# Optimization experiments

Hardware: AMD Instinct MI355X
Metric: run time of the kernel (lower is better)

The kernel has to match this reference:

```python
import jax, jax.numpy as jnp
import numpy as np

N_NODES = 50000
N_EDGES = 1600000
N_OBS = 128
HIDDEN = 128
N_ACT = 32
K_OUT = 64


def gcn_conv(x, W, b, src, dst, n_nodes):
    """PyG GCNConv: out = D^{-1/2} (A + I) D^{-1/2} (x W) + b.

    Self-loop handled analytically (norm = 1/deg for the loop edge)
    instead of concatenating loop edges.
    """
    h = x @ W  # [N, out]
    # degree with self loops: in-degree + 1
    deg = jnp.zeros((n_nodes,), x.dtype).at[dst].add(jnp.ones((), x.dtype)) + 1.0
    dinv = jax.lax.rsqrt(deg)  # deg >= 1, safe
    norm = dinv[src] * dinv[dst]  # [E]
    agg = jax.ops.segment_sum(h[src] * norm[:, None], dst, num_segments=n_nodes)
    agg = agg + h * (dinv * dinv)[:, None]  # self-loop term: h / deg
    return agg + b


def setup_inputs() -> dict:
    key = jax.random.key(0)
    ks = jax.random.split(key, 6)
    x = jax.random.normal(ks[0], (N_OBS, N_NODES), dtype=jnp.float32)
    edge_index = jax.random.randint(ks[1], (2, N_EDGES), 0, N_NODES, dtype=jnp.int64)
    onehot_values = jax.random.uniform(ks[2], (K_OUT, N_NODES), dtype=jnp.float32)
    W1 = jax.random.normal(ks[3], (N_OBS, HIDDEN), dtype=jnp.float32) / np.sqrt(N_OBS)
    b1 = jnp.zeros((HIDDEN,), jnp.float32)
    W2 = jax.random.normal(ks[4], (HIDDEN, N_ACT), dtype=jnp.float32) / np.sqrt(HIDDEN)
    b2 = jnp.zeros((N_ACT,), jnp.float32)
    return {"x": x, "edge_index": edge_index, "onehot_values": onehot_values,
            "W1": W1, "b1": b1, "W2": W2, "b2": b2}


def reference(x, edge_index, onehot_values, W1, b1, W2, b2):
    # eval mode: dropout is identity
    src, dst = edge_index[0], edge_index[1]
    h = x.T  # graph.x.T -> [N, n_obs]
    h = jax.nn.relu(gcn_conv(h, W1, b1, src, dst, N_NODES))
    h = gcn_conv(h, W2, b2, src, dst, N_NODES)
    return onehot_values @ h  # [K_OUT, N_ACT]
```

## Files before the change

kernel.cpp:

```cpp
#include <hip/hip_runtime.h>

#define NN 50000
#define NE 1600000
#define NB 98
#define BSH 9
#define BCAP 17408

#define OFF_H1    0
#define OFF_AGG1  3200000
#define OFF_HW2   9600000
#define OFF_AGG2  10400000
#define OFF_DINV  12000000
#define OFF_ROWS  12050000
#define OFF_GCNT  12101000
#define OFF_GBASE 12101200
#define OFF_CSRC  12102000
#define OFF_BIN   13702000

typedef __attribute__((ext_vector_type(8))) short bf16x8;
typedef __attribute__((ext_vector_type(8))) unsigned short u16x8;
typedef __attribute__((ext_vector_type(4))) float f32x4;

__device__ __forceinline__ unsigned short f2b(float f) {
    unsigned u = __float_as_uint(f);
    u += 0x7fffu + ((u >> 16) & 1u);
    return (unsigned short)(u >> 16);
}
__device__ __forceinline__ float b2f(unsigned short h) {
    return __uint_as_float((unsigned)h << 16);
}
__device__ __forceinline__ float blo(unsigned u) { return __uint_as_float(u << 16); }
__device__ __forceinline__ float bhi(unsigned u) { return __uint_as_float(u & 0xffff0000u); }

__global__ __launch_bounds__(256) void k_binA(const int* __restrict__ ei,
                                              int* __restrict__ gcount,
                                              unsigned* __restrict__ binned) {
    __shared__ int hist[NB];
    const int t = threadIdx.x;
    if (t < NB) hist[t] = 0;
    __syncthreads();
    const int e0 = blockIdx.x * (NE / 256);
    const int e1 = e0 + (NE / 256);
    for (int e = e0 + t; e < e1; e += 256)
        atomicAdd(&hist[ei[NE + e] >> BSH], 1);
    __syncthreads();
    if (t < NB) {
        const int v = hist[t];
        hist[t] = atomicAdd(&gcount[t], v);
    }
    __syncthreads();
    for (int e = e0 + t; e < e1; e += 256) {
        const int s = ei[e], d = ei[NE + e];
        const int b = d >> BSH;
        const int pos = atomicAdd(&hist[b], 1);
        binned[(size_t)b * BCAP + pos] = (unsigned)s | ((unsigned)(d & 511) << 16);
    }
}

__global__ __launch_bounds__(128) void k_base(const int* __restrict__ gcount,
                                              int* __restrict__ gbase) {
    __shared__ int s[128];
    const int t = threadIdx.x;
    const int v = (t < NB) ? gcount[t] : 0;
    s[t] = v;
    __syncthreads();
    #pragma unroll
    for (int off = 1; off < 128; off <<= 1) {
        const int x = (t >= off) ? s[t - off] : 0;
        __syncthreads();
        s[t] += x;
        __syncthreads();
    }
    if (t < NB) gbase[t] = s[t] - v;
    if (t == NB - 1) gbase[NB] = s[t];
}

__global__ __launch_bounds__(256) void k_binB(const int* __restrict__ gcount,
                                              const int* __restrict__ gbase,
                                              const unsigned* __restrict__ binned,
                                              int* __restrict__ rows,
                                              float* __restrict__ dinv,
                                              int* __restrict__ csrc) {
    __shared__ int deg[512];
    __shared__ int off[512];
    __shared__ int partial[256];
    const int b = blockIdx.x, t = threadIdx.x;
    const int n0 = b << BSH;
    const int nloc = (NN - n0 < 512) ? (NN - n0) : 512;
    const int cnt = gcount[b];
    const int obase = gbase[b];
    const unsigned* eb = binned + (size_t)b * BCAP;
    deg[t] = 0;
    deg[t + 256] = 0;
    __syncthreads();
    for (int i = t; i < cnt; i += 256) atomicAdd(&deg[eb[i] >> 16], 1);
    __syncthreads();
    const int s0 = deg[2 * t], s1 = deg[2 * t + 1];
    partial[t] = s0 + s1;
    __syncthreads();
    #pragma unroll
    for (int o = 1; o < 256; o <<= 1) {
        const int x = (t >= o) ? partial[t - o] : 0;
        __syncthreads();
        partial[t] += x;
        __syncthreads();
    }
    const int ep = partial[t] - (s0 + s1);
    off[2 * t] = ep;
    off[2 * t + 1] = ep + s0;
    __syncthreads();
    for (int i = t; i < nloc; i += 256) {
        rows[n0 + i] = obase + off[i];
        dinv[n0 + i] = rsqrtf((float)deg[i] + 1.0f);
    }
    if (b == NB - 1 && t == 0) rows[NN] = NE;
    __syncthreads();
    for (int i = t; i < cnt; i += 256) {
        const unsigned r = eb[i];
        const int local = atomicAdd(&off[r >> 16], 1);
        csrc[obase + local] = (int)(r & 0xffffu);
    }
}

__global__ __launch_bounds__(256) void k_w1t(const float* __restrict__ W1,
                                             unsigned short* __restrict__ w1t) {
    const int id = blockIdx.x * 1024 + threadIdx.x;
    #pragma unroll
    for (int i = 0; i < 4; ++i) {
        const int e = id + 256 * i;
        const int k = e >> 7, c = e & 127;
        w1t[c * 128 + k] = f2b(W1[e]);
    }
}

__global__ __launch_bounds__(256) void k_gemm1(const float* __restrict__ x,
                                               const unsigned short* __restrict__ w1t,
                                               const float* __restrict__ dinv,
                                               unsigned short* __restrict__ h1s) {
    __shared__ unsigned short lxs[64 * 136];
    const int t = threadIdx.x;
    const int gn0 = blockIdx.x * 64;
    {
        const int col = t & 63, kr = t >> 6;
        const int gn = gn0 + col;
        #pragma unroll
        for (int i = 0; i < 4; ++i) {
            const int k0 = kr * 32 + i * 8;
            u16x8 v;
            #pragma unroll
            for (int j = 0; j < 8; ++j) {
                const float xv = (gn < NN) ? x[(size_t)(k0 + j) * NN + gn] : 0.f;
                v[j] = f2b(xv);
            }
            *(u16x8*)&lxs[col * 136 + k0] = v;
        }
    }
    __syncthreads();
    const int w = t >> 6, l = t & 63;
    const int lr = l & 15, lg = l >> 4;
    const unsigned short* pa = &lxs[(w * 16 + lr) * 136 + lg * 8];
    f32x4 acc[8];
    #pragma unroll
    for (int ct = 0; ct < 8; ++ct) acc[ct] = (f32x4){0.f, 0.f, 0.f, 0.f};
    #pragma unroll
    for (int ks = 0; ks < 4; ++ks) {
        const bf16x8 av = *(const bf16x8*)&pa[ks * 32];
        const unsigned short* pw = &w1t[lr * 128 + ks * 32 + lg * 8];
        const bf16x8 b0 = *(const bf16x8*)&pw[0 * 16 * 128];
        const bf16x8 b1 = *(const bf16x8*)&pw[1 * 16 * 128];
        const bf16x8 b2 = *(const bf16x8*)&pw[2 * 16 * 128];
        const bf16x8 b3 = *(const bf16x8*)&pw[3 * 16 * 128];
        const bf16x8 b4 = *(const bf16x8*)&pw[4 * 16 * 128];
        const bf16x8 b5 = *(const bf16x8*)&pw[5 * 16 * 128];
        const bf16x8 b6 = *(const bf16x8*)&pw[6 * 16 * 128];
        const bf16x8 b7 = *(const bf16x8*)&pw[7 * 16 * 128];
        acc[0] = __builtin_amdgcn_mfma_f32_16x16x32_bf16(av, b0, acc[0], 0, 0, 0);
        acc[1] = __builtin_amdgcn_mfma_f32_16x16x32_bf16(av, b1, acc[1], 0, 0, 0);
        acc[2] = __builtin_amdgcn_mfma_f32_16x16x32_bf16(av, b2, acc[2], 0, 0, 0);
        acc[3] = __builtin_amdgcn_mfma_f32_16x16x32_bf16(av, b3, acc[3], 0, 0, 0);
        acc[4] = __builtin_amdgcn_mfma_f32_16x16x32_bf16(av, b4, acc[4], 0, 0, 0);
        acc[5] = __builtin_amdgcn_mfma_f32_16x16x32_bf16(av, b5, acc[5], 0, 0, 0);
        acc[6] = __builtin_amdgcn_mfma_f32_16x16x32_bf16(av, b6, acc[6], 0, 0, 0);
        acc[7] = __builtin_amdgcn_mfma_f32_16x16x32_bf16(av, b7, acc[7], 0, 0, 0);
    }
    __syncthreads();
    const int nl0 = w * 16 + lg * 4;
    const float4 dv = *(const float4*)&dinv[gn0 + nl0];
    const float dva[4] = {dv.x, dv.y, dv.z, dv.w};
    #pragma unroll
    for (int ct = 0; ct < 8; ++ct) {
        const int c = ct * 16 + lr;
        #pragma unroll
        for (int r = 0; r < 4; ++r)
            lxs[(nl0 + r) * 136 + c] = f2b(acc[ct][r] * dva[r]);
    }
    __syncthreads();
    {
        const int row = t >> 2, cb = (t & 3) * 32;
        const int gn = gn0 + row;
        if (gn < NN) {
            #pragma unroll
            for (int i = 0; i < 4; ++i)
                *(u16x8*)&h1s[(size_t)gn * 128 + cb + i * 8] =
                    *(const u16x8*)&lxs[row * 136 + cb + i * 8];
        }
    }
}

__global__ __launch_bounds__(256) void k_gather1(const int* __restrict__ rows,
                                                 const int* __restrict__ csrc,
                                                 const float* __restrict__ dinv,
                                                 const unsigned short* __restrict__ h1s,
                                                 unsigned short* __restrict__ ag1b) {
    const int n = __builtin_amdgcn_readfirstlane((blockIdx.x * 256 + threadIdx.x) >> 6);
    const int lane = threadIdx.x & 63;
    if (n >= NN) return;
    const int beg = rows[n], end = rows[n + 1];
    float ax0 = 0.f, ay0 = 0.f, ax1 = 0.f, ay1 = 0.f;
    float ax2 = 0.f, ay2 = 0.f, ax3 = 0.f, ay3 = 0.f;
    int p = beg;
    for (; p + 16 <= end; p += 16) {
        const int s0 = csrc[p + 0], s1 = csrc[p + 1], s2 = csrc[p + 2], s3 = csrc[p + 3];
        const int s4 = csrc[p + 4], s5 = csrc[p + 5], s6 = csrc[p + 6], s7 = csrc[p + 7];
        const int s8 = csrc[p + 8], s9 = csrc[p + 9], sa = csrc[p + 10], sb = csrc[p + 11];
        const int sc = csrc[p + 12], sd = csrc[p + 13], se = csrc[p + 14], sf = csrc[p + 15];
        const unsigned u0 = *(const unsigned*)&h1s[(size_t)s0 * 128 + lane * 2];
        const unsigned u1 = *(const unsigned*)&h1s[(size_t)s1 * 128 + lane * 2];
        const unsigned u2 = *(const unsigned*)&h1s[(size_t)s2 * 128 + lane * 2];
        const unsigned u3 = *(const unsigned*)&h1s[(size_t)s3 * 128 + lane * 2];
        const unsigned u4 = *(const unsigned*)&h1s[(size_t)s4 * 128 + lane * 2];
        const unsigned u5 = *(const unsigned*)&h1s[(size_t)s5 * 128 + lane * 2];
        const unsigned u6 = *(const unsigned*)&h1s[(size_t)s6 * 128 + lane * 2];
        const unsigned u7 = *(const unsigned*)&h1s[(size_t)s7 * 128 + lane * 2];
        const unsigned u8 = *(const unsigned*)&h1s[(size_t)s8 * 128 + lane * 2];
        const unsigned u9 = *(const unsigned*)&h1s[(size_t)s9 * 128 + lane * 2];
        const unsigned ua = *(const unsigned*)&h1s[(size_t)sa * 128 + lane * 2];
        const unsigned ub = *(const unsigned*)&h1s[(size_t)sb * 128 + lane * 2];
        const unsigned uc = *(const unsigned*)&h1s[(size_t)sc * 128 + lane * 2];
        const unsigned ud = *(const unsigned*)&h1s[(size_t)sd * 128 + lane * 2];
        const unsigned ue = *(const unsigned*)&h1s[(size_t)se * 128 + lane * 2];
        const unsigned uf = *(const unsigned*)&h1s[(size_t)sf * 128 + lane * 2];
        ax0 += blo(u0); ay0 += bhi(u0);
        ax1 += blo(u1); ay1 += bhi(u1);
        ax2 += blo(u2); ay2 += bhi(u2);
        ax3 += blo(u3); ay3 += bhi(u3);
        ax0 += blo(u4); ay0 += bhi(u4);
        ax1 += blo(u5); ay1 += bhi(u5);
        ax2 += blo(u6); ay2 += bhi(u6);
        ax3 += blo(u7); ay3 += bhi(u7);
        ax0 += blo(u8); ay0 += bhi(u8);
        ax1 += blo(u9); ay1 += bhi(u9);
        ax2 += blo(ua); ay2 += bhi(ua);
        ax3 += blo(ub); ay3 += bhi(ub);
        ax0 += blo(uc); ay0 += bhi(uc);
        ax1 += blo(ud); ay1 += bhi(ud);
        ax2 += blo(ue); ay2 += bhi(ue);
        ax3 += blo(uf); ay3 += bhi(uf);
    }
    for (; p + 4 <= end; p += 4) {
        const int s0 = csrc[p + 0], s1 = csrc[p + 1], s2 = csrc[p + 2], s3 = csrc[p + 3];
        const unsigned u0 = *(const unsigned*)&h1s[(size_t)s0 * 128 + lane * 2];
        const unsigned u1 = *(const unsigned*)&h1s[(size_t)s1 * 128 + lane * 2];
        const unsigned u2 = *(const unsigned*)&h1s[(size_t)s2 * 128 + lane * 2];
        const unsigned u3 = *(const unsigned*)&h1s[(size_t)s3 * 128 + lane * 2];
        ax0 += blo(u0); ay0 += bhi(u0);
        ax1 += blo(u1); ay1 += bhi(u1);
        ax2 += blo(u2); ay2 += bhi(u2);
        ax3 += blo(u3); ay3 += bhi(u3);
    }
    for (; p < end; ++p) {
        const int s = csrc[p];
        const unsigned u0 = *(const unsigned*)&h1s[(size_t)s * 128 + lane * 2];
        ax0 += blo(u0); ay0 += bhi(u0);
    }
    const float dn = dinv[n];
    const float sx = ((ax0 + ax1) + (ax2 + ax3)) * dn;
    const float sy = ((ay0 + ay1) + (ay2 + ay3)) * dn;
    const unsigned pk = (unsigned)f2b(sx) | ((unsigned)f2b(sy) << 16);
    *(unsigned*)&ag1b[(size_t)n * 128 + lane * 2] = pk;
}

__global__ __launch_bounds__(256) void k_fuse1(const unsigned short* __restrict__ ag1b,
                                               const unsigned short* __restrict__ h1s,
                                               const float* __restrict__ dinv,
                                               const float* __restrict__ b1,
                                               const float* __restrict__ W2,
                                               unsigned short* __restrict__ hw2s) {
    __shared__ float hs[32][132];
    __shared__ float w2s[128 * 32];
    const int t = threadIdx.x;
    const int n0 = blockIdx.x * 32;
    #pragma unroll
    for (int i = 0; i < 16; ++i) w2s[t + 256 * i] = W2[t + 256 * i];
    #pragma unroll
    for (int i = 0; i < 4; ++i) {
        const int idx4 = t + 256 * i;
        const int n = idx4 >> 5, c4 = (idx4 & 31) * 4;
        const int node = n0 + n;
        float4 r = make_float4(0.f, 0.f, 0.f, 0.f);
        if (node < NN) {
            const ushort4 au = *(const ushort4*)&ag1b[(size_t)node * 128 + c4];
            const ushort4 hu = *(const ushort4*)&h1s[(size_t)node * 128 + c4];
            const float dn = dinv[node];
            const float4 bb = *(const float4*)&b1[c4];
            r.x = fmaxf(fmaf(b2f(hu.x), dn, b2f(au.x)) + bb.x, 0.f);
            r.y = fmaxf(fmaf(b2f(hu.y), dn, b2f(au.y)) + bb.y, 0.f);
            r.z = fmaxf(fmaf(b2f(hu.z), dn, b2f(au.z)) + bb.z, 0.f);
            r.w = fmaxf(fmaf(b2f(hu.w), dn, b2f(au.w)) + bb.w, 0.f);
        }
        *(float4*)&hs[n][c4] = r;
    }
    __syncthreads();
    const int n = t >> 3, j4 = (t & 7) * 4;
    const int node = n0 + n;
    float acc[4] = {0.f, 0.f, 0.f, 0.f};
    #pragma unroll 8
    for (int k = 0; k < 128; ++k) {
        const float hv = hs[n][k];
        const float4 wv = *(const float4*)&w2s[k * 32 + j4];
        acc[0] = fmaf(hv, wv.x, acc[0]);
        acc[1] = fmaf(hv, wv.y, acc[1]);
        acc[2] = fmaf(hv, wv.z, acc[2]);
        acc[3] = fmaf(hv, wv.w, acc[3]);
    }
    if (node < NN) {
        const float ds = dinv[node];
        ushort4 pk;
        pk.x = f2b(acc[0] * ds); pk.y = f2b(acc[1] * ds);
        pk.z = f2b(acc[2] * ds); pk.w = f2b(acc[3] * ds);
        *(ushort4*)&hw2s[(size_t)node * 32 + j4] = pk;
    }
}

__global__ __launch_bounds__(256) void k_gather2(const int* __restrict__ rows,
                                                 const int* __restrict__ csrc,
                                                 const float* __restrict__ dinv,
                                                 const unsigned short* __restrict__ hw2s,
                                                 float* __restrict__ agg2) {
    const int n = __builtin_amdgcn_readfirstlane((blockIdx.x * 256 + threadIdx.x) >> 6);
    const int lane = threadIdx.x & 63;
    const int j = lane & 31;
    const int hi = lane >> 5;
    if (n >= NN) return;
    const int beg = rows[n], end = rows[n + 1];
    float a0 = 0.f, a1 = 0.f, a2 = 0.f, a3 = 0.f;
    float a4 = 0.f, a5 = 0.f, a6 = 0.f, a7 = 0.f;
    int p = beg;
    for (; p + 16 <= end; p += 16) {
        const int e0 = csrc[p + 0 + hi],  e1 = csrc[p + 2 + hi];
        const int e2 = csrc[p + 4 + hi],  e3 = csrc[p + 6 + hi];
        const int e4 = csrc[p + 8 + hi],  e5 = csrc[p + 10 + hi];
        const int e6 = csrc[p + 12 + hi], e7 = csrc[p + 14 + hi];
        const unsigned short v0 = hw2s[(size_t)e0 * 32 + j];
        const unsigned short v1 = hw2s[(size_t)e1 * 32 + j];
        const unsigned short v2 = hw2s[(size_t)e2 * 32 + j];
        const unsigned short v3 = hw2s[(size_t)e3 * 32 + j];
        const unsigned short v4 = hw2s[(size_t)e4 * 32 + j];
        const unsigned short v5 = hw2s[(size_t)e5 * 32 + j];
        const unsigned short v6 = hw2s[(size_t)e6 * 32 + j];
        const unsigned short v7 = hw2s[(size_t)e7 * 32 + j];
        a0 += b2f(v0); a1 += b2f(v1); a2 += b2f(v2); a3 += b2f(v3);
        a4 += b2f(v4); a5 += b2f(v5); a6 += b2f(v6); a7 += b2f(v7);
    }
    for (; p + 2 <= end; p += 2) {
        const int e = csrc[p + hi];
        a0 += b2f(hw2s[(size_t)e * 32 + j]);
    }
    if (p < end) {
        if (!hi) {
            const int e = csrc[p];
            a0 += b2f(hw2s[(size_t)e * 32 + j]);
        }
    }
    float sum = ((a0 + a1) + (a2 + a3)) + ((a4 + a5) + (a6 + a7));
    sum += __shfl_xor(sum, 32);
    if (!hi) agg2[(size_t)n * 32 + j] = sum * dinv[n];
}

__global__ __launch_bounds__(256) void k_final(const float* __restrict__ O,
                                               const float* __restrict__ agg2,
                                               const unsigned short* __restrict__ hw2s,
                                               const float* __restrict__ dinv,
                                               const float* __restrict__ b2,
                                               float* __restrict__ out) {
    __shared__ float h2s[128][32];
    __shared__ float Os[64][128];
    const int t = threadIdx.x;
    const int n0 = blockIdx.x * 128;
    #pragma unroll
    for (int i = 0; i < 16; ++i) {
        const int idx = t + 256 * i;
        const int n = idx >> 5, j = idx & 31;
        const int node = n0 + n;
        float v = 0.f;
        if (node < NN) {
            const float dn = dinv[node];
            v = fmaf(b2f(hw2s[(size_t)node * 32 + j]), dn,
                     agg2[(size_t)node * 32 + j]) + b2[j];
        }
        h2s[n][j] = v;
    }
    #pragma unroll
    for (int i = 0; i < 32; ++i) {
        const int idx = t + 256 * i;
        const int r = idx >> 7, c = idx & 127;
        const int node = n0 + c;
        Os[r][c] = (node < NN) ? O[(size_t)r * NN + node] : 0.f;
    }
    __syncthreads();
    const int j = t & 31, k0 = (t >> 5) * 8;
    float acc[8];
    #pragma unroll
    for (int i = 0; i < 8; ++i) acc[i] = 0.f;
    for (int n = 0; n < 128; ++n) {
        const float hv = h2s[n][j];
        #pragma unroll
        for (int i = 0; i < 8; ++i) acc[i] = fmaf(Os[k0 + i][n], hv, acc[i]);
    }
    #pragma unroll
    for (int i = 0; i < 8; ++i) atomicAdd(&out[(k0 + i) * 32 + j], acc[i]);
}

extern "C" void kernel_launch(void* const* d_in, const int* in_sizes, int n_in,
                              void* d_out, int out_size, void* d_ws, size_t ws_size,
                              hipStream_t stream) {
    const float* x  = (const float*)d_in[0];
    const int*   ei = (const int*)d_in[1];
    const float* O  = (const float*)d_in[2];
    const float* W1 = (const float*)d_in[3];
    const float* b1 = (const float*)d_in[4];
    const float* W2 = (const float*)d_in[5];
    const float* b2 = (const float*)d_in[6];
    float* out = (float*)d_out;

    float* wsf = (float*)d_ws;
    unsigned short* h1s  = (unsigned short*)(wsf + OFF_H1);
    unsigned short* ag1b = (unsigned short*)(wsf + OFF_AGG1);
    unsigned short* hw2s = (unsigned short*)(wsf + OFF_HW2);
    float*          agg2 = wsf + OFF_AGG2;
    float* dinv  = wsf + OFF_DINV;
    int*   rows  = (int*)(wsf + OFF_ROWS);
    int*   gcnt  = (int*)(wsf + OFF_GCNT);
    int*   gbase = (int*)(wsf + OFF_GBASE);
    int*   csrc  = (int*)(wsf + OFF_CSRC);
    unsigned* binned = (unsigned*)(wsf + OFF_BIN);
    unsigned short* w1t = (unsigned short*)(wsf + OFF_BIN);

    hipMemsetAsync(gcnt, 0, NB * 4, stream);

    k_binA<<<256, 256, 0, stream>>>(ei, gcnt, binned);
    k_base<<<1, 128, 0, stream>>>(gcnt, gbase);
    k_binB<<<NB, 256, 0, stream>>>(gcnt, gbase, binned, rows, dinv, csrc);

    k_w1t<<<16, 256, 0, stream>>>(W1, w1t);
    k_gemm1<<<(NN + 63) / 64, 256, 0, stream>>>(x, w1t, dinv, h1s);
    k_gather1<<<(NN * 64 + 255) / 256, 256, 0, stream>>>(rows, csrc, dinv, h1s, ag1b);
    k_fuse1<<<(NN + 31) / 32, 256, 0, stream>>>(ag1b, h1s, dinv, b1, W2, hw2s);
    k_gather2<<<(NN * 64 + 255) / 256, 256, 0, stream>>>(rows, csrc, dinv, hw2s, agg2);

    hipMemsetAsync(out, 0, (size_t)out_size * 4, stream);
    k_final<<<(NN + 127) / 128, 256, 0, stream>>>(O, agg2, hw2s, dinv, b2, out);
}
```

Measured before the change: 219.4 us.

## Store CSR sources as 16-bit and split layer-1 gather into column halves

CSR source indices are stored as unsigned shorts and read as packed pairs, so each half-wave takes alternate edges. This halves the index bandwidth in both gathers. The layer-1 gather is split into two launches, each covering 64 feature columns with a cross-half shuffle reduction, to shrink the per-pass working set. The cost is an extra launch, indices read twice, and the assumption that node ids fit in 16 bits.

```diff
diff --git a/kernel.cpp b/kernel.cpp
--- a/kernel.cpp
+++ b/kernel.cpp
@@ -80,7 +80,7 @@
                                               const unsigned* __restrict__ binned,
                                               int* __restrict__ rows,
                                               float* __restrict__ dinv,
-                                              int* __restrict__ csrc) {
+                                              unsigned short* __restrict__ csrc) {
     __shared__ int deg[512];
     __shared__ int off[512];
     __shared__ int partial[256];
@@ -118,7 +118,7 @@
     for (int i = t; i < cnt; i += 256) {
         const unsigned r = eb[i];
         const int local = atomicAdd(&off[r >> 16], 1);
-        csrc[obase + local] = (int)(r & 0xffffu);
+        csrc[obase + local] = (unsigned short)(r & 0xffffu);
     }
 }
 
@@ -208,76 +208,82 @@
 }
 
 __global__ __launch_bounds__(256) void k_gather1(const int* __restrict__ rows,
-                                                 const int* __restrict__ csrc,
+                                                 const unsigned short* __restrict__ csrc,
                                                  const float* __restrict__ dinv,
                                                  const unsigned short* __restrict__ h1s,
-                                                 unsigned short* __restrict__ ag1b) {
+                                                 unsigned short* __restrict__ ag1b,
+                                                 const int coff) {
     const int n = __builtin_amdgcn_readfirstlane((blockIdx.x * 256 + threadIdx.x) >> 6);
     const int lane = threadIdx.x & 63;
     if (n >= NN) return;
+    const int j2 = (lane & 31) * 2;
+    const int hi = lane >> 5;
     const int beg = rows[n], end = rows[n + 1];
-    float ax0 = 0.f, ay0 = 0.f, ax1 = 0.f, ay1 = 0.f;
-    float ax2 = 0.f, ay2 = 0.f, ax3 = 0.f, ay3 = 0.f;
+    float a0x = 0.f, a0y = 0.f, a1x = 0.f, a1y = 0.f;
+    float a2x = 0.f, a2y = 0.f, a3x = 0.f, a3y = 0.f;
     int p = beg;
+    if ((p & 1) && p < end) {
+        if (!hi) {
+            const int s = csrc[p];
+            const unsigned u = *(const unsigned*)&h1s[(size_t)s * 128 + coff + j2];
+            a0x += blo(u); a0y += bhi(u);
+        }
+        ++p;
+    }
     for (; p + 16 <= end; p += 16) {
-        const int s0 = csrc[p + 0], s1 = csrc[p + 1], s2 = csrc[p + 2], s3 = csrc[p + 3];
-        const int s4 = csrc[p + 4], s5 = csrc[p + 5], s6 = csrc[p + 6], s7 = csrc[p + 7];
-        const int s8 = csrc[p + 8], s9 = csrc[p + 9], sa = csrc[p + 10], sb = csrc[p + 11];
-        const int sc = csrc[p + 12], sd = csrc[p + 13], se = csrc[p + 14], sf = csrc[p + 15];
-        const unsigned u0 = *(const unsigned*)&h1s[(size_t)s0 * 128 + lane * 2];
-        const unsigned u1 = *(const unsigned*)&h1s[(size_t)s1 * 128 + lane * 2];
-        const unsigned u2 = *(const unsigned*)&h1s[(size_t)s2 * 128 + lane * 2];
-        const unsigned u3 = *(const unsigned*)&h1s[(size_t)s3 * 128 + lane * 2];
-        const unsigned u4 = *(const unsigned*)&h1s[(size_t)s4 * 128 + lane * 2];
-        const unsigned u5 = *(const unsigned*)&h1s[(size_t)s5 * 128 + lane * 2];
-        const unsigned u6 = *(const unsigned*)&h1s[(size_t)s6 * 128 + lane * 2];
-        const unsigned u7 = *(const unsigned*)&h1s[(size_t)s7 * 128 + lane * 2];
-        const unsigned u8 = *(const unsigned*)&h1s[(size_t)s8 * 128 + lane * 2];
-        const unsigned u9 = *(const unsigned*)&h1s[(size_t)s9 * 128 + lane * 2];
-        const unsigned ua = *(const unsigned*)&h1s[(size_t)sa * 128 + lane * 2];
-        const unsigned ub = *(const unsigned*)&h1s[(size_t)sb * 128 + lane * 2];
-        const unsigned uc = *(const unsigned*)&h1s[(size_t)sc * 128 + lane * 2];
-        const unsigned ud = *(const unsigned*)&h1s[(size_t)sd * 128 + lane * 2];
-        const unsigned ue = *(const unsigned*)&h1s[(size_t)se * 128 + lane * 2];
-        const unsigned uf = *(const unsigned*)&h1s[(size_t)sf * 128 + lane * 2];
-        ax0 += blo(u0); ay0 += bhi(u0);
-        ax1 += blo(u1); ay1 += bhi(u1);
-        ax2 += blo(u2); ay2 += bhi(u2);
-        ax3 += blo(u3); ay3 += bhi(u3);
-        ax0 += blo(u4); ay0 += bhi(u4);
-        ax1 += blo(u5); ay1 += bhi(u5);
-        ax2 += blo(u6); ay2 += bhi(u6);
-        ax3 += blo(u7); ay3 += bhi(u7);
-        ax0 += blo(u8); ay0 += bhi(u8);
-        ax1 += blo(u9); ay1 += bhi(u9);
-        ax2 += blo(ua); ay2 += bhi(ua);
-        ax3 += blo(ub); ay3 += bhi(ub);
-        ax0 += blo(uc); ay0 += bhi(uc);
-        ax1 += blo(ud); ay1 += bhi(ud);
-        ax2 += blo(ue); ay2 += bhi(ue);
-        ax3 += blo(uf); ay3 += bhi(uf);
-    }
-    for (; p + 4 <= end; p += 4) {
-        const int s0 = csrc[p + 0], s1 = csrc[p + 1], s2 = csrc[p + 2], s3 = csrc[p + 3];
-        const unsigned u0 = *(const unsigned*)&h1s[(size_t)s0 * 128 + lane * 2];
-        const unsigned u1 = *(const unsigned*)&h1s[(size_t)s1 * 128 + lane * 2];
-        const unsigned u2 = *(const unsigned*)&h1s[(size_t)s2 * 128 + lane * 2];
-        const unsigned u3 = *(const unsigned*)&h1s[(size_t)s3 * 128 + lane * 2];
-        ax0 += blo(u0); ay0 += bhi(u0);
-        ax1 += blo(u1); ay1 += bhi(u1);
-        ax2 += blo(u2); ay2 += bhi(u2);
-        ax3 += blo(u3); ay3 += bhi(u3);
-    }
-    for (; p < end; ++p) {
+        const unsigned d0 = *(const unsigned*)&csrc[p + 0];
+        const unsigned d1 = *(const unsigned*)&csrc[p + 2];
+        const unsigned d2 = *(const unsigned*)&csrc[p + 4];
+        const unsigned d3 = *(const unsigned*)&csrc[p + 6];
+        const unsigned d4 = *(const unsigned*)&csrc[p + 8];
+        const unsigned d5 = *(const unsigned*)&csrc[p + 10];
+        const unsigned d6 = *(const unsigned*)&csrc[p + 12];
+        const unsigned d7 = *(const unsigned*)&csrc[p + 14];
+        const int s0 = hi ? (int)(d0 >> 16) : (int)(d0 & 0xffffu);
+        const int s1 = hi ? (int)(d1 >> 16) : (int)(d1 & 0xffffu);
+        const int s2 = hi ? (int)(d2 >> 16) : (int)(d2 & 0xffffu);
+        const int s3 = hi ? (int)(d3 >> 16) : (int)(d3 & 0xffffu);
+        const int s4 = hi ? (int)(d4 >> 16) : (int)(d4 & 0xffffu);
+        const int s5 = hi ? (int)(d5 >> 16) : (int)(d5 & 0xffffu);
+        const int s6 = hi ? (int)(d6 >> 16) : (int)(d6 & 0xffffu);
+        const int s7 = hi ? (int)(d7 >> 16) : (int)(d7 & 0xffffu);
+        const unsigned u0 = *(const unsigned*)&h1s[(size_t)s0 * 128 + coff + j2];
+        const unsigned u1 = *(const unsigned*)&h1s[(size_t)s1 * 128 + coff + j2];
+        const unsigned u2 = *(const unsigned*)&h1s[(size_t)s2 * 128 + coff + j2];
+        const unsigned u3 = *(const unsigned*)&h1s[(size_t)s3 * 128 + coff + j2];
+        const unsigned u4 = *(const unsigned*)&h1s[(size_t)s4 * 128 + coff + j2];
+        const unsigned u5 = *(const unsigned*)&h1s[(size_t)s5 * 128 + coff + j2];
+        const unsigned u6 = *(const unsigned*)&h1s[(size_t)s6 * 128 + coff + j2];
+        const unsigned u7 = *(const unsigned*)&h1s[(size_t)s7 * 128 + coff + j2];
+        a0x += blo(u0); a0y += bhi(u0);
+        a1x += blo(u1); a1y += bhi(u1);
+        a2x += blo(u2); a2y += bhi(u2);
+        a3x += blo(u3); a3y += bhi(u3);
+        a0x += blo(u4); a0y += bhi(u4);
+        a1x += blo(u5); a1y += bhi(u5);
+        a2x += blo(u6); a2y += bhi(u6);
+        a3x += blo(u7); a3y += bhi(u7);
+    }
+    for (; p + 2 <= end; p += 2) {
+        const unsigned d = *(const unsigned*)&csrc[p];
+        const int s = hi ? (int)(d >> 16) : (int)(d & 0xffffu);
+        const unsigned u = *(const unsigned*)&h1s[(size_t)s * 128 + coff + j2];
+        a0x += blo(u); a0y += bhi(u);
+    }
+    if (p < end && !hi) {
         const int s = csrc[p];
-        const unsigned u0 = *(const unsigned*)&h1s[(size_t)s * 128 + lane * 2];
-        ax0 += blo(u0); ay0 += bhi(u0);
-    }
-    const float dn = dinv[n];
-    const float sx = ((ax0 + ax1) + (ax2 + ax3)) * dn;
-    const float sy = ((ay0 + ay1) + (ay2 + ay3)) * dn;
-    const unsigned pk = (unsigned)f2b(sx) | ((unsigned)f2b(sy) << 16);
-    *(unsigned*)&ag1b[(size_t)n * 128 + lane * 2] = pk;
+        const unsigned u = *(const unsigned*)&h1s[(size_t)s * 128 + coff + j2];
+        a0x += blo(u); a0y += bhi(u);
+    }
+    float sx = (a0x + a1x) + (a2x + a3x);
+    float sy = (a0y + a1y) + (a2y + a3y);
+    sx += __shfl_xor(sx, 32);
+    sy += __shfl_xor(sy, 32);
+    if (lane < 32) {
+        const float dn = dinv[n];
+        const unsigned pk = (unsigned)f2b(sx * dn) | ((unsigned)f2b(sy * dn) << 16);
+        *(unsigned*)&ag1b[(size_t)n * 128 + coff + j2] = pk;
+    }
 }
 
 __global__ __launch_bounds__(256) void k_fuse1(const unsigned short* __restrict__ ag1b,
@@ -333,7 +339,7 @@
 }
 
 __global__ __launch_bounds__(256) void k_gather2(const int* __restrict__ rows,
-                                                 const int* __restrict__ csrc,
+                                                 const unsigned short* __restrict__ csrc,
                                                  const float* __restrict__ dinv,
                                                  const unsigned short* __restrict__ hw2s,
                                                  float* __restrict__ agg2) {
@@ -346,11 +352,27 @@
     float a0 = 0.f, a1 = 0.f, a2 = 0.f, a3 = 0.f;
     float a4 = 0.f, a5 = 0.f, a6 = 0.f, a7 = 0.f;
     int p = beg;
+    if ((p & 1) && p < end) {
+        if (!hi) a0 += b2f(hw2s[(size_t)csrc[p] * 32 + j]);
+        ++p;
+    }
     for (; p + 16 <= end; p += 16) {
-        const int e0 = csrc[p + 0 + hi],  e1 = csrc[p + 2 + hi];
-        const int e2 = csrc[p + 4 + hi],  e3 = csrc[p + 6 + hi];
-        const int e4 = csrc[p + 8 + hi],  e5 = csrc[p + 10 + hi];
-        const int e6 = csrc[p + 12 + hi], e7 = csrc[p + 14 + hi];
+        const unsigned d0 = *(const unsigned*)&csrc[p + 0];
+        const unsigned d1 = *(const unsigned*)&csrc[p + 2];
+        const unsigned d2 = *(const unsigned*)&csrc[p + 4];
+        const unsigned d3 = *(const unsigned*)&csrc[p + 6];
+        const unsigned d4 = *(const unsigned*)&csrc[p + 8];
+        const unsigned d5 = *(const unsigned*)&csrc[p + 10];
+        const unsigned d6 = *(const unsigned*)&csrc[p + 12];
+        const unsigned d7 = *(const unsigned*)&csrc[p + 14];
+        const int e0 = hi ? (int)(d0 >> 16) : (int)(d0 & 0xffffu);
+        const int e1 = hi ? (int)(d1 >> 16) : (int)(d1 & 0xffffu);
+        const int e2 = hi ? (int)(d2 >> 16) : (int)(d2 & 0xffffu);
+        const int e3 = hi ? (int)(d3 >> 16) : (int)(d3 & 0xffffu);
+        const int e4 = hi ? (int)(d4 >> 16) : (int)(d4 & 0xffffu);
+        const int e5 = hi ? (int)(d5 >> 16) : (int)(d5 & 0xffffu);
+        const int e6 = hi ? (int)(d6 >> 16) : (int)(d6 & 0xffffu);
+        const int e7 = hi ? (int)(d7 >> 16) : (int)(d7 & 0xffffu);
         const unsigned short v0 = hw2s[(size_t)e0 * 32 + j];
         const unsigned short v1 = hw2s[(size_t)e1 * 32 + j];
         const unsigned short v2 = hw2s[(size_t)e2 * 32 + j];
@@ -363,14 +385,12 @@
         a4 += b2f(v4); a5 += b2f(v5); a6 += b2f(v6); a7 += b2f(v7);
     }
     for (; p + 2 <= end; p += 2) {
-        const int e = csrc[p + hi];
+        const unsigned d = *(const unsigned*)&csrc[p];
+        const int e = hi ? (int)(d >> 16) : (int)(d & 0xffffu);
         a0 += b2f(hw2s[(size_t)e * 32 + j]);
     }
-    if (p < end) {
-        if (!hi) {
-            const int e = csrc[p];
-            a0 += b2f(hw2s[(size_t)e * 32 + j]);
-        }
+    if (p < end && !hi) {
+        a0 += b2f(hw2s[(size_t)csrc[p] * 32 + j]);
     }
     float sum = ((a0 + a1) + (a2 + a3)) + ((a4 + a5) + (a6 + a7));
     sum += __shfl_xor(sum, 32);
@@ -442,7 +462,7 @@
     int*   rows  = (int*)(wsf + OFF_ROWS);
     int*   gcnt  = (int*)(wsf + OFF_GCNT);
     int*   gbase = (int*)(wsf + OFF_GBASE);
-    int*   csrc  = (int*)(wsf + OFF_CSRC);
+    unsigned short* csrc = (unsigned short*)(wsf + OFF_CSRC);
     unsigned* binned = (unsigned*)(wsf + OFF_BIN);
     unsigned short* w1t = (unsigned short*)(wsf + OFF_BIN);
 
@@ -454,7 +474,8 @@
 
     k_w1t<<<16, 256, 0, stream>>>(W1, w1t);
     k_gemm1<<<(NN + 63) / 64, 256, 0, stream>>>(x, w1t, dinv, h1s);
-    k_gather1<<<(NN * 64 + 255) / 256, 256, 0, stream>>>(rows, csrc, dinv, h1s, ag1b);
+    k_gather1<<<(NN * 64 + 255) / 256, 256, 0, stream>>>(rows, csrc, dinv, h1s, ag1b, 0);
+    k_gather1<<<(NN * 64 + 255) / 256, 256, 0, stream>>>(rows, csrc, dinv, h1s, ag1b, 64);
     k_fuse1<<<(NN + 31) / 32, 256, 0, stream>>>(ag1b, h1s, dinv, b1, W2, hw2s);
     k_gather2<<<(NN * 64 + 255) / 256, 256, 0, stream>>>(rows, csrc, dinv, hw2s, agg2);
 
```

After: 231.0 us. 5.2% more time.
